# Kernel tuning notes

Measured on AMD Instinct MI355X. Metric: run time of the kernel, lower is better.

The kernel has to match this reference:

```python
import jax, jax.numpy as jnp
import numpy as np

B_, L, DM = 2, 1024, 1024
D_STATE, D_CONV, EXPAND = 16, 4, 2
DI = EXPAND * DM          # 2048 inner dim
DTR = DM // 16            # 64 dt rank


def setup_inputs() -> dict:
    key = jax.random.key(0)
    ks = jax.random.split(key, 16)
    g = lambda k, shp, s: jax.random.normal(k, shp, jnp.float32) * s
    inp = {
        "x": g(ks[0], (B_, L, DM), 1.0),
        "ln_g": jnp.ones((DM,), jnp.float32),
        "ln_b": jnp.zeros((DM,), jnp.float32),
        "in_proj_w": g(ks[1], (2 * DI, DM), (2.0 / (DM + 2 * DI)) ** 0.5),
        "conv_w": g(ks[2], (DI, 1, D_CONV), (2.0 / D_CONV) ** 0.5),
        "conv_b": jnp.zeros((DI,), jnp.float32),
        "dtin_w": g(ks[3], (DTR, DI), (2.0 / (DI + DTR)) ** 0.5),
        "dtin_b": jnp.zeros((DTR,), jnp.float32),
        "dt_w": g(ks[4], (DI, DTR), DTR ** -0.5),
        "dt_b": jnp.log(jnp.expm1(jax.random.uniform(ks[5], (DI,), jnp.float32, 1e-3, 0.1))),  # inverse-softplus of dt in [dt_min, dt_max]
        "B_w": g(ks[6], (D_STATE, DI), DI ** -0.5),
        "C_w": g(ks[7], (D_STATE, DI), DI ** -0.5),
        "A_log": jnp.log(jnp.broadcast_to(jnp.arange(1, D_STATE + 1, dtype=jnp.float32), (DI, D_STATE))),
        "D": jnp.ones((DI,), jnp.float32),
        "out_w": g(ks[8], (DM, DI), (2.0 / (DM + DI)) ** 0.5),
    }
    return inp


def _layernorm(x, g, b, eps=1e-5):
    mu = jnp.mean(x, -1, keepdims=True)
    var = jnp.mean(jnp.square(x - mu), -1, keepdims=True)
    return (x - mu) * jax.lax.rsqrt(var + eps) * g + b


def _selective_scan(u, dt, Bm, Cm, A, Dp):
    # u,dt: (b,l,di); Bm,Cm: (b,l,n); A: (di,n)
    def step(h, inp):
        dt_t, B_t, C_t, u_t = inp  # (b,di),(b,n),(b,n),(b,di)
        dA = jnp.exp(dt_t[..., None] * A)                       # (b,di,n)
        h = h * dA + (dt_t * u_t)[..., None] * B_t[:, None, :]   # (b,di,n)
        y = jnp.einsum("bdn,bn->bd", h, C_t)
        return h, y

    tm = lambda a: jnp.swapaxes(a, 0, 1)  # time-major
    h0 = jnp.zeros((u.shape[0], u.shape[2], A.shape[1]), u.dtype)
    _, ys = jax.lax.scan(step, h0, (tm(dt), tm(Bm), tm(Cm), tm(u)))
    return jnp.swapaxes(ys, 0, 1) + u * Dp  # (b,l,di)


def reference(x, ln_g, ln_b, in_proj_w, conv_w, conv_b, dtin_w, dtin_b,
              dt_w, dt_b, B_w, C_w, A_log, D, out_w):
    residual = x
    xn = _layernorm(x, ln_g, ln_b)
    xz = xn @ in_proj_w.T                       # (b,l,2*di)
    x_proj, z = jnp.split(xz, 2, axis=-1)
    # causal depthwise conv1d (left pad d_conv-1, truncate to seq_len)
    xp = jnp.pad(x_proj, ((0, 0), (D_CONV - 1, 0), (0, 0)))
    x_conv = conv_b
    for k in range(D_CONV):
        x_conv = x_conv + conv_w[:, 0, k] * xp[:, k:k + L, :]
    x_conv = jax.nn.silu(x_conv)
    dt_in = x_conv @ dtin_w.T + dtin_b          # (b,l,dtr)
    dt = jax.nn.softplus(dt_in @ dt_w.T + dt_b) # (b,l,di)
    Bm = x_conv @ B_w.T                         # (b,l,n)
    Cm = x_conv @ C_w.T
    A = -jnp.exp(A_log)                         # (di,n)
    y = _selective_scan(x_conv, dt, Bm, Cm, A, D)
    y = y * jax.nn.silu(z)
    return y @ out_w.T + residual
```

## Files before the change

kernel.cpp:

```cpp
#include <hip/hip_runtime.h>
#include <hip/hip_bf16.h>
#include <cstdint>

#define BL    2
#define LSEQ  1024
#define DMOD  1024
#define DIN   2048
#define NST   16
#define DTRK  64
#define MR    (BL*LSEQ)

#define CCH 16
#define TCH 64
#define KSPLIT 8

typedef __bf16 bf16x8 __attribute__((ext_vector_type(8)));
typedef float  f32x4  __attribute__((ext_vector_type(4)));

#if __has_builtin(__builtin_amdgcn_exp2f)
#define EXP2F(x) __builtin_amdgcn_exp2f(x)
#else
#define EXP2F(x) exp2f(x)
#endif
#define LOG2E 1.4426950408889634f

__device__ __forceinline__ void glds16(const void* g, const void* l) {
    __builtin_amdgcn_global_load_lds(
        (__attribute__((address_space(1))) void*)(uintptr_t)(g),
        (__attribute__((address_space(3))) void*)(uint32_t)(uintptr_t)(l),
        16, 0, 0);
}

__device__ __forceinline__ __bf16 f2b(float f) {
    __hip_bfloat16 t = __float2bfloat16(f);
    return *(__bf16*)&t;
}

template <int MODE, int TM, int TN, int BK>
__global__ __launch_bounds__(256, 3) void gemm_bt(
    const __hip_bfloat16* __restrict__ A, int lda,
    const __hip_bfloat16* __restrict__ Bw, int ldb,
    int M, int N, int Ksl,
    void* __restrict__ e0, void* __restrict__ e1,
    const float* __restrict__ bias, const float* __restrict__ bias2,
    const float* __restrict__ Af)
{
    constexpr bool FUSE = (MODE == 0);
    static_assert(!FUSE || BK == 64, "fused conv epilogue assumes BK=64");
    static_assert(MODE != 2 || BK == 64, "MODE 2 staging assumes BK=64");
    constexpr int WM = TM / 2, WN = TN / 2;
    constexpr int MT = WM / 16, NT = WN / 16;
    constexpr int C8 = BK / 8;
    constexpr int RPP = 256 / C8;
    constexpr int PA = TM / RPP, PB = TN / RPP;
    __shared__ __align__(16) __hip_bfloat16 sA[2][TM * BK];
    __shared__ __align__(16) __hip_bfloat16 sB[2][TN * BK];
    __shared__ __align__(16) __hip_bfloat16 sH[2][(FUSE ? 16 : 1) * 64];

    auto SW = [](int row) { return (BK == 32) ? ((row >> 1) & 3) : (row & 7); };

    int bx = blockIdx.x, by = blockIdx.y;
    if ((gridDim.y & 7) == 0) {
        const int bid = blockIdx.x + gridDim.x * blockIdx.y;
        const int xcd = bid & 7, s = bid >> 3;
        bx = s % gridDim.x;
        by = (s / gridDim.x) * 8 + xcd;
    }
    const int m0 = by * TM;
    const int n0 = bx * TN;
    const int k0 = blockIdx.z * Ksl;
    const int tid = threadIdx.x;
    const int w = tid >> 6, lane = tid & 63;
    const int wm = (w >> 1) * WM, wn = (w & 1) * WN;
    const int lrow = lane & 15, lq = lane >> 4;

    const int r0 = tid / C8;
    const int q = ((tid % C8) - SW(r0)) & (C8 - 1);
    const __hip_bfloat16* pa[PA];
    const __hip_bfloat16* pb[PB];
    if constexpr (MODE != 2) {
#pragma unroll
        for (int p = 0; p < PA; p++) pa[p] = A + (size_t)(m0 + r0 + RPP * p) * lda + k0 + q * 8;
    }
#pragma unroll
    for (int p = 0; p < PB; p++) pb[p] = Bw + (size_t)(n0 + r0 + RPP * p) * ldb + k0 + q * 8;

    auto stageA2 = [&](int buf, int kb) {
        if constexpr (MODE == 2) {
#pragma unroll
            for (int p = 0; p < PA; p++) {
                const int rr = r0 + RPP * p;
                const float* src = Af + (size_t)(m0 + rr) * 64 + kb * BK + q * 8;
                const float4 f0 = *(const float4*)src;
                const float4 f1 = *(const float4*)(src + 4);
                const float4 b0 = *(const float4*)&bias2[q * 8];
                const float4 b1 = *(const float4*)&bias2[q * 8 + 4];
                bf16x8 o;
                o[0] = f2b(f0.x + b0.x); o[1] = f2b(f0.y + b0.y);
                o[2] = f2b(f0.z + b0.z); o[3] = f2b(f0.w + b0.w);
                o[4] = f2b(f1.x + b1.x); o[5] = f2b(f1.y + b1.y);
                o[6] = f2b(f1.z + b1.z); o[7] = f2b(f1.w + b1.w);
                *(bf16x8*)&sA[buf][(tid + 256 * p) * 8] = o;
            }
        }
    };

    const bool isX = FUSE && (n0 < DIN);
    const __hip_bfloat16* ph = nullptr;
    if (FUSE) {
        const int rh = tid >> 3;
        const int qh = ((tid & 7) - (rh & 7)) & 7;
        ph = A + (size_t)(m0 - 16 + rh) * lda + k0 + qh * 8;
    }

    f32x4 acc[MT][NT];
#pragma unroll
    for (int i = 0; i < MT; i++)
#pragma unroll
        for (int j = 0; j < NT; j++) { acc[i][j][0]=0.f; acc[i][j][1]=0.f; acc[i][j][2]=0.f; acc[i][j][3]=0.f; }
    f32x4 hacc[FUSE ? NT : 1];
    if (FUSE)
#pragma unroll
        for (int j = 0; j < NT; j++) { hacc[j][0]=0.f; hacc[j][1]=0.f; hacc[j][2]=0.f; hacc[j][3]=0.f; }

    const int nk = Ksl / BK;
    if constexpr (MODE == 2) stageA2(0, 0);
    else {
#pragma unroll
        for (int p = 0; p < PA; p++) glds16(pa[p], &sA[0][(tid + 256 * p) * 8]);
    }
#pragma unroll
    for (int p = 0; p < PB; p++) glds16(pb[p], &sB[0][(tid + 256 * p) * 8]);
    if (isX && tid < 128) glds16(ph, &sH[0][tid * 8]);

    for (int kb = 0; kb < nk; ++kb) {
        const int cur = kb & 1, nxt = cur ^ 1;
        __syncthreads();
        if (kb + 1 < nk) {
            if constexpr (MODE == 2) stageA2(nxt, kb + 1);
            else {
#pragma unroll
                for (int p = 0; p < PA; p++) { pa[p] += BK; glds16(pa[p], &sA[nxt][(tid + 256 * p) * 8]); }
            }
#pragma unroll
            for (int p = 0; p < PB; p++) { pb[p] += BK; glds16(pb[p], &sB[nxt][(tid + 256 * p) * 8]); }
            if (isX && tid < 128) { ph += BK; glds16(ph, &sH[nxt][tid * 8]); }
        }
#pragma unroll
        for (int s = 0; s < BK / 32; s++) {
            bf16x8 af[MT], bb[NT];
#pragma unroll
            for (int mt = 0; mt < MT; mt++) {
                const int row = wm + mt * 16 + lrow;
                const int pc = ((s * 4 + lq) + SW(row)) & (C8 - 1);
                af[mt] = *(const bf16x8*)&sA[cur][row * BK + pc * 8];
            }
#pragma unroll
            for (int nt = 0; nt < NT; nt++) {
                const int row = wn + nt * 16 + lrow;
                const int pc = ((s * 4 + lq) + SW(row)) & (C8 - 1);
                bb[nt] = *(const bf16x8*)&sB[cur][row * BK + pc * 8];
            }
#pragma unroll
            for (int mt = 0; mt < MT; mt++)
#pragma unroll
                for (int nt = 0; nt < NT; nt++)
                    acc[mt][nt] = __builtin_amdgcn_mfma_f32_16x16x32_bf16(af[mt], bb[nt], acc[mt][nt], 0, 0, 0);
            if (isX && w < 2) {
                const int pcH = ((s * 4 + lq) + (lrow & 7)) & 7;
                const bf16x8 afh = *(const bf16x8*)&sH[cur][lrow * 64 + pcH * 8];
#pragma unroll
                for (int nt = 0; nt < NT; nt++)
                    hacc[nt] = __builtin_amdgcn_mfma_f32_16x16x32_bf16(afh, bb[nt], hacc[nt], 0, 0, 0);
            }
        }
    }

    if (MODE == 0 && isX) {
        __syncthreads();
        __hip_bfloat16* tile = (__hip_bfloat16*)&sB[0][0];
        constexpr int TS = TN + 8;
#pragma unroll
        for (int mt = 0; mt < MT; mt++)
#pragma unroll
            for (int nt = 0; nt < NT; nt++) {
                const int col = wn + nt * 16 + lrow;
#pragma unroll
                for (int r = 0; r < 4; r++)
                    tile[(16 + wm + mt * 16 + lq * 4 + r) * TS + col] = __float2bfloat16(acc[mt][nt][r]);
            }
        if (w < 2) {
#pragma unroll
            for (int nt = 0; nt < NT; nt++) {
                const int col = wn + nt * 16 + lrow;
#pragma unroll
                for (int r = 0; r < 4; r++)
                    tile[(lq * 4 + r) * TS + col] = __float2bfloat16(hacc[nt][r]);
            }
        }
        __syncthreads();
        const int c2 = (tid & 63) * 2;
        const int rg = tid >> 6;
        const int dg = n0 + c2;
        const float4 wA = *(const float4*)&bias[dg * 4];
        const float4 wB = *(const float4*)&bias[dg * 4 + 4];
        const float cbA = bias2[dg], cbB = bias2[dg + 1];
        const int l0 = m0 & (LSEQ - 1);
        const int rbase = rg * 16;
        float a0, a1, a2, b0, b1, b2;
        if (l0 == 0 && rg == 0) {
            a0 = a1 = a2 = b0 = b1 = b2 = 0.f;
        } else {
            const int hr = 16 + rbase - 3;
            a0 = __bfloat162float(tile[(hr + 0) * TS + c2]);
            b0 = __bfloat162float(tile[(hr + 0) * TS + c2 + 1]);
            a1 = __bfloat162float(tile[(hr + 1) * TS + c2]);
            b1 = __bfloat162float(tile[(hr + 1) * TS + c2 + 1]);
            a2 = __bfloat162float(tile[(hr + 2) * TS + c2]);
            b2 = __bfloat162float(tile[(hr + 2) * TS + c2 + 1]);
        }
        __hip_bfloat16* xcbp = (__hip_bfloat16*)e0;
#pragma unroll 4
        for (int i = 0; i < 16; i++) {
            const int row = rbase + i;
            const float a3 = __bfloat162float(tile[(16 + row) * TS + c2]);
            const float b3 = __bfloat162float(tile[(16 + row) * TS + c2 + 1]);
            float sa = cbA + wA.x * a0 + wA.y * a1 + wA.z * a2 + wA.w * a3;
            float sb = cbB + wB.x * b0 + wB.y * b1 + wB.z * b2 + wB.w * b3;
            sa = sa / (1.f + __expf(-sa));
            sb = sb / (1.f + __expf(-sb));
            __hip_bfloat16 ha = __float2bfloat16(sa), hb = __float2bfloat16(sb);
            ushort2 o;
            o.x = (unsigned short)__hip_bfloat16_raw(ha).x;
            o.y = (unsigned short)__hip_bfloat16_raw(hb).x;
            *(ushort2*)&xcbp[(size_t)(m0 + row) * DIN + dg] = o;
            a0 = a1; a1 = a2; a2 = a3;
            b0 = b1; b1 = b2; b2 = b3;
        }
        return;
    }
#pragma unroll
    for (int mt = 0; mt < MT; mt++) {
#pragma unroll
        for (int nt = 0; nt < NT; nt++) {
            const int gn = n0 + wn + nt * 16 + lrow;
            if (gn >= N) continue;
            const int gmb = m0 + wm + mt * 16 + lq * 4;
#pragma unroll
            for (int r = 0; r < 4; r++) {
                const int gm = gmb + r;
                const float v = acc[mt][nt][r];
                if (MODE == 0) {
                    const float s = v / (1.f + __expf(-v));
                    ((__hip_bfloat16*)e1)[(size_t)gm * DIN + (gn - DIN)] = __float2bfloat16(s);
                } else if (MODE == 1) {
                    if (gn < 64)      atomicAdd((float*)e0 + (size_t)gm * 64 + gn, v);
                    else if (gn < 80) atomicAdd((float*)e1 + (size_t)gm * NST + (gn - 64), v);
                    else              atomicAdd((float*)e1 + (size_t)MR * NST + (size_t)gm * NST + (gn - 80), v);
                } else if (MODE == 2) {
                    const float xx = v + bias[gn];
                    const float sp = (xx > 20.f) ? xx : log1pf(__expf(xx));
                    ((__hip_bfloat16*)e0)[(size_t)gm * N + gn] = __float2bfloat16(sp);
                } else {
                    ((float*)e0)[(size_t)gm * N + gn] = v + ((const float*)e1)[(size_t)gm * N + gn];
                }
            }
        }
    }
}

#define NCVT 1654784
#define NZR  49152
__global__ void prep_kernel(const float* __restrict__ x, const float* __restrict__ ln_g,
                            const float* __restrict__ ln_b,
                            const float* __restrict__ w_in, const float* __restrict__ dtin_w,
                            const float* __restrict__ B_w, const float* __restrict__ C_w,
                            const float* __restrict__ dt_w, const float* __restrict__ out_w,
                            __hip_bfloat16* __restrict__ w1b, __hip_bfloat16* __restrict__ wpb,
                            __hip_bfloat16* __restrict__ dtwb, __hip_bfloat16* __restrict__ owb,
                            __hip_bfloat16* __restrict__ xn, float* __restrict__ zblock)
{
    const int b = blockIdx.x;
    const int tid = threadIdx.x;
    if (b < MR) {
        const float4 v = ((const float4*)(x + (size_t)b * DMOD))[tid];
        float s  = v.x + v.y + v.z + v.w;
        float sq = v.x * v.x + v.y * v.y + v.z * v.z + v.w * v.w;
#pragma unroll
        for (int off = 32; off >= 1; off >>= 1) {
            s  += __shfl_down(s, off, 64);
            sq += __shfl_down(sq, off, 64);
        }
        __shared__ float red[8];
        const int w = tid >> 6, lane = tid & 63;
        if (lane == 0) { red[w] = s; red[4 + w] = sq; }
        __syncthreads();
        s  = red[0] + red[1] + red[2] + red[3];
        sq = red[4] + red[5] + red[6] + red[7];
        const float mean = s * (1.f / DMOD);
        const float rstd = rsqrtf(sq * (1.f / DMOD) - mean * mean + 1e-5f);
        const int col = tid * 4;
        const float vv[4] = {v.x, v.y, v.z, v.w};
#pragma unroll
        for (int i = 0; i < 4; i++)
            xn[(size_t)b * DMOD + col + i] =
                __float2bfloat16((vv[i] - mean) * rstd * ln_g[col + i] + ln_b[col + i]);
        return;
    }
    const int nb = gridDim.x - MR;
    for (int v4 = (b - MR) * 256 + tid; v4 < NCVT + NZR; v4 += nb * 256) {
        if (v4 >= NCVT) {
            float4 z; z.x = z.y = z.z = z.w = 0.f;
            ((float4*)zblock)[v4 - NCVT] = z;
            continue;
        }
        const int i = v4 * 4;
        const float* s; __hip_bfloat16* dk;
        if      (i < 4194304) { s = w_in   + i;             dk = w1b  + i; }
        else if (i < 4325376) { s = dtin_w + (i - 4194304); dk = wpb  + (i - 4194304); }
        else if (i < 4358144) { s = B_w    + (i - 4325376); dk = wpb  + 131072 + (i - 4325376); }
        else if (i < 4390912) { s = C_w    + (i - 4358144); dk = wpb  + 163840 + (i - 4358144); }
        else if (i < 4521984) { s = dt_w   + (i - 4390912); dk = dtwb + (i - 4390912); }
        else                  { s = out_w  + (i - 4521984); dk = owb  + (i - 4521984); }
        const float4 f = *(const float4*)s;
        ushort4 o;
        o.x = (unsigned short)(__hip_bfloat16_raw(__float2bfloat16(f.x)).x);
        o.y = (unsigned short)(__hip_bfloat16_raw(__float2bfloat16(f.y)).x);
        o.z = (unsigned short)(__hip_bfloat16_raw(__float2bfloat16(f.z)).x);
        o.w = (unsigned short)(__hip_bfloat16_raw(__float2bfloat16(f.w)).x);
        *(ushort4*)dk = o;
    }
}


__global__ __launch_bounds__(256) void scan_p1(
    const __hip_bfloat16* __restrict__ dt, const __hip_bfloat16* __restrict__ u,
    const float* __restrict__ Bm, const float* __restrict__ A_log,
    float* __restrict__ Aprod, float* __restrict__ Bacc)
{
    __shared__ float sB[TCH * NST];
    const int blk = blockIdx.x;
    const int bb = blk / (CCH * 16), c = (blk >> 4) & (CCH - 1), dtile = blk & 15;
    const int tid = threadIdx.x;
    const int nh = tid & 1, dl = tid >> 1;
    const int d = dtile * 128 + dl;
    const int row0 = bb * LSEQ + c * TCH;

#pragma unroll
    for (int k = 0; k < (TCH * NST) / 256; k++)
        sB[tid + 256 * k] = Bm[(size_t)row0 * NST + tid + 256 * k];
    __syncthreads();

    float a2[8];
    {
        const float4 al0 = *(const float4*)&A_log[(size_t)d * NST + nh * 8];
        const float4 al1 = *(const float4*)&A_log[(size_t)d * NST + nh * 8 + 4];
        a2[0] = -__expf(al0.x) * LOG2E; a2[1] = -__expf(al0.y) * LOG2E;
        a2[2] = -__expf(al0.z) * LOG2E; a2[3] = -__expf(al0.w) * LOG2E;
        a2[4] = -__expf(al1.x) * LOG2E; a2[5] = -__expf(al1.y) * LOG2E;
        a2[6] = -__expf(al1.z) * LOG2E; a2[7] = -__expf(al1.w) * LOG2E;
    }
    const __hip_bfloat16* pdt = dt + (size_t)row0 * DIN + d;
    const __hip_bfloat16* pu  = u  + (size_t)row0 * DIN + d;
    float h[8], Ap[8];
#pragma unroll
    for (int j = 0; j < 8; j++) { h[j] = 0.f; Ap[j] = 1.f; }

#pragma unroll 4
    for (int t = 0; t < TCH; t++) {
        const float dtv = __bfloat162float(pdt[t * DIN]);
        const float uv  = __bfloat162float(pu[t * DIN]);
        const float du = dtv * uv;
        float bv[8];
        *(float4*)&bv[0] = *(const float4*)&sB[t * NST + nh * 8];
        *(float4*)&bv[4] = *(const float4*)&sB[t * NST + nh * 8 + 4];
#pragma unroll
        for (int j = 0; j < 8; j++) {
            const float e = EXP2F(dtv * a2[j]);
            Ap[j] *= e;
            h[j] = h[j] * e + du * bv[j];
        }
    }
    const size_t idx = (((size_t)bb * CCH + c) * DIN + d) * NST + nh * 8;
    *(float4*)&Aprod[idx]     = make_float4(Ap[0], Ap[1], Ap[2], Ap[3]);
    *(float4*)&Aprod[idx + 4] = make_float4(Ap[4], Ap[5], Ap[6], Ap[7]);
    *(float4*)&Bacc[idx]      = make_float4(h[0], h[1], h[2], h[3]);
    *(float4*)&Bacc[idx + 4]  = make_float4(h[4], h[5], h[6], h[7]);
}

__global__ __launch_bounds__(256) void scan_p2(
    const float* __restrict__ Aprod, const float* __restrict__ Bacc,
    float* __restrict__ hstart)
{
    const int i = blockIdx.x * 256 + threadIdx.x;
    const int bb = i >> 15;
    const int dn = i & 32767;
    const size_t base = (((size_t)bb * CCH) << 15) + dn;
    float ap[CCH], bc[CCH];
#pragma unroll
    for (int c = 0; c < CCH; c++) {
        ap[c] = Aprod[base + ((size_t)c << 15)];
        bc[c] = Bacc[base + ((size_t)c << 15)];
    }
    float hs = 0.f;
#pragma unroll
    for (int c = 0; c < CCH; c++) {
        hstart[base + ((size_t)c << 15)] = hs;
        hs = fmaf(ap[c], hs, bc[c]);
    }
}

__global__ __launch_bounds__(256) void scan_p3(
    const __hip_bfloat16* __restrict__ dt, const __hip_bfloat16* __restrict__ u,
    const float* __restrict__ Bm, const float* __restrict__ Cm,
    const float* __restrict__ A_log, const float* __restrict__ Dp,
    const __hip_bfloat16* __restrict__ zs, const float* __restrict__ hstart,
    __hip_bfloat16* __restrict__ y)
{
    __shared__ float sB[TCH * NST], sC[TCH * NST];
    const int blk = blockIdx.x;
    const int bb = blk / (CCH * 16), c = (blk >> 4) & (CCH - 1), dtile = blk & 15;
    const int tid = threadIdx.x;
    const int nh = tid & 1, dl = tid >> 1;
    const int d = dtile * 128 + dl;
    const int row0 = bb * LSEQ + c * TCH;

#pragma unroll
    for (int k = 0; k < (TCH * NST) / 256; k++) {
        sB[tid + 256 * k] = Bm[(size_t)row0 * NST + tid + 256 * k];
        sC[tid + 256 * k] = Cm[(size_t)row0 * NST + tid + 256 * k];
    }
    __syncthreads();

    float a2[8];
    {
        const float4 al0 = *(const float4*)&A_log[(size_t)d * NST + nh * 8];
        const float4 al1 = *(const float4*)&A_log[(size_t)d * NST + nh * 8 + 4];
        a2[0] = -__expf(al0.x) * LOG2E; a2[1] = -__expf(al0.y) * LOG2E;
        a2[2] = -__expf(al0.z) * LOG2E; a2[3] = -__expf(al0.w) * LOG2E;
        a2[4] = -__expf(al1.x) * LOG2E; a2[5] = -__expf(al1.y) * LOG2E;
        a2[6] = -__expf(al1.z) * LOG2E; a2[7] = -__expf(al1.w) * LOG2E;
    }
    const float Dd = Dp[d];
    const size_t idx = (((size_t)bb * CCH + c) * DIN + d) * NST + nh * 8;
    float h[8];
    *(float4*)&h[0] = *(const float4*)&hstart[idx];
    *(float4*)&h[4] = *(const float4*)&hstart[idx + 4];

    const __hip_bfloat16* pdt = dt + (size_t)row0 * DIN + d;
    const __hip_bfloat16* pu  = u  + (size_t)row0 * DIN + d;
    const __hip_bfloat16* pz  = zs + (size_t)row0 * DIN + d;
    __hip_bfloat16* py = y + (size_t)row0 * DIN + d;

#pragma unroll 2
    for (int t = 0; t < TCH; t++) {
        const float dtv = __bfloat162float(pdt[t * DIN]);
        const float uv  = __bfloat162float(pu[t * DIN]);
        const float du = dtv * uv;
        float bv[8], cv[8];
        *(float4*)&bv[0] = *(const float4*)&sB[t * NST + nh * 8];
        *(float4*)&bv[4] = *(const float4*)&sB[t * NST + nh * 8 + 4];
        *(float4*)&cv[0] = *(const float4*)&sC[t * NST + nh * 8];
        *(float4*)&cv[4] = *(const float4*)&sC[t * NST + nh * 8 + 4];
        float yp = 0.f;
#pragma unroll
        for (int j = 0; j < 8; j++) {
            const float e = EXP2F(dtv * a2[j]);
            h[j] = h[j] * e + du * bv[j];
            yp += h[j] * cv[j];
        }
        yp += __shfl_xor(yp, 1, 64);
        if (nh == 0) {
            const float zv = __bfloat162float(pz[t * DIN]);
            py[t * DIN] = __float2bfloat16((yp + uv * Dd) * zv);
        }
    }
}

extern "C" void kernel_launch(void* const* d_in, const int* in_sizes, int n_in,
                              void* d_out, int out_size, void* d_ws, size_t ws_size,
                              hipStream_t stream) {
    const float* x      = (const float*)d_in[0];
    const float* ln_g   = (const float*)d_in[1];
    const float* ln_b   = (const float*)d_in[2];
    const float* w_in   = (const float*)d_in[3];
    const float* conv_w = (const float*)d_in[4];
    const float* conv_b = (const float*)d_in[5];
    const float* dtin_w = (const float*)d_in[6];
    const float* dtin_b = (const float*)d_in[7];
    const float* dt_w   = (const float*)d_in[8];
    const float* dt_b   = (const float*)d_in[9];
    const float* B_w    = (const float*)d_in[10];
    const float* C_w    = (const float*)d_in[11];
    const float* A_log  = (const float*)d_in[12];
    const float* Dp     = (const float*)d_in[13];
    const float* out_w  = (const float*)d_in[14];
    float* out = (float*)d_out;

    char* ws = (char*)d_ws;
    auto alloc = [&](size_t bytes) { char* p = ws; ws += (bytes + 255) & ~255ull; return p; };
    __hip_bfloat16* w1b   = (__hip_bfloat16*)alloc((size_t)4096 * 1024 * 2);
    __hip_bfloat16* wpb   = (__hip_bfloat16*)alloc((size_t)96 * 2048 * 2);
    __hip_bfloat16* dtwb  = (__hip_bfloat16*)alloc((size_t)2048 * 64 * 2);
    __hip_bfloat16* owb   = (__hip_bfloat16*)alloc((size_t)1024 * 2048 * 2);
    __hip_bfloat16* xnb   = (__hip_bfloat16*)alloc((size_t)MR * DMOD * 2);
    __hip_bfloat16* zs    = (__hip_bfloat16*)alloc((size_t)MR * DIN * 2);
    __hip_bfloat16* xcb   = (__hip_bfloat16*)alloc((size_t)MR * DIN * 2);
    __hip_bfloat16* dtb   = (__hip_bfloat16*)alloc((size_t)MR * DIN * 2);
    __hip_bfloat16* yb    = (__hip_bfloat16*)alloc((size_t)MR * DIN * 2);
    float*          zblock= (float*)alloc((size_t)196608 * 4);
    float*          Aprod = (float*)alloc((size_t)BL * CCH * DIN * NST * 4);
    float*          Bacc  = (float*)alloc((size_t)BL * CCH * DIN * NST * 4);
    float*          hstart= (float*)alloc((size_t)BL * CCH * DIN * NST * 4);

    float* fdtin = zblock;
    float* Bmf   = zblock + 131072;

    prep_kernel<<<MR + 896, 256, 0, stream>>>(x, ln_g, ln_b, w_in, dtin_w, B_w, C_w, dt_w,
                                              out_w, w1b, wpb, dtwb, owb, xnb, zblock);

    gemm_bt<0, 64, 128, 64><<<dim3(32, 32, 1), 256, 0, stream>>>(
        xnb, 1024, w1b, 1024, MR, 4096, 1024, xcb, zs, conv_w, conv_b, nullptr);

    gemm_bt<1, 64, 128, 64><<<dim3(1, 32, KSPLIT), 256, 0, stream>>>(
        xcb, 2048, wpb, 2048, MR, 96, 2048 / KSPLIT, fdtin, Bmf, nullptr, nullptr, nullptr);

    gemm_bt<2, 64, 128, 64><<<dim3(16, 32, 1), 256, 0, stream>>>(
        nullptr, 0, dtwb, 64, MR, DIN, 64, dtb, nullptr, dt_b, dtin_b, fdtin);

    scan_p1<<<BL * CCH * 16, 256, 0, stream>>>(dtb, xcb, Bmf, A_log, Aprod, Bacc);
    scan_p2<<<BL * DIN * NST / 256, 256, 0, stream>>>(Aprod, Bacc, hstart);
    scan_p3<<<BL * CCH * 16, 256, 0, stream>>>(dtb, xcb, Bmf, Bmf + (size_t)MR * NST,
                                               A_log, Dp, zs, hstart, yb);

    gemm_bt<3, 64, 64, 64><<<dim3(16, 32, 1), 256, 0, stream>>>(
        yb, 2048, owb, 2048, MR, DMOD, 2048, out, (void*)x, nullptr, nullptr, nullptr);
}
```

Before: 247.9 us.

## Stage scan dt/u/z tiles in LDS and shorten chunk length in chunked scan

The scan kernels now copy the per-chunk dt, u and z tiles into shared memory with async global-to-LDS 16-byte loads, instead of each thread doing strided 2-byte global loads every timestep. Outputs y are gathered in LDS and written back as coalesced 16-byte vector stores. The chunk length goes from 64 to 32 and the chunk count from 16 to 32, which doubles the blocks for more parallelism but lengthens the sequential cross-chunk prefix pass. The barrier is moved after the A_log/hstart loads so that latency overlaps the async copies.

Result: faster. 222.0 us (-10.4%).

```diff
diff --git a/kernel.cpp b/kernel.cpp
--- a/kernel.cpp
+++ b/kernel.cpp
@@ -10,8 +10,8 @@
 #define DTRK  64
 #define MR    (BL*LSEQ)
 
-#define CCH 16
-#define TCH 64
+#define CCH 32
+#define TCH 32
 #define KSPLIT 8
 
 typedef __bf16 bf16x8 __attribute__((ext_vector_type(8)));
@@ -339,17 +339,29 @@
     float* __restrict__ Aprod, float* __restrict__ Bacc)
 {
     __shared__ float sB[TCH * NST];
+    __shared__ __align__(16) __hip_bfloat16 sDT[TCH * 128];
+    __shared__ __align__(16) __hip_bfloat16 sU [TCH * 128];
     const int blk = blockIdx.x;
     const int bb = blk / (CCH * 16), c = (blk >> 4) & (CCH - 1), dtile = blk & 15;
     const int tid = threadIdx.x;
     const int nh = tid & 1, dl = tid >> 1;
     const int d = dtile * 128 + dl;
+    const int d0 = dtile * 128;
     const int row0 = bb * LSEQ + c * TCH;
 
+    {
+        const int r = tid >> 4, cq = (tid & 15) * 8;
+        const __hip_bfloat16* gdt = dt + (size_t)row0 * DIN + d0;
+        const __hip_bfloat16* gu  = u  + (size_t)row0 * DIN + d0;
+#pragma unroll
+        for (int p = 0; p < TCH / 16; p++) {
+            glds16(gdt + (size_t)(r + 16 * p) * DIN + cq, &sDT[(r + 16 * p) * 128 + cq]);
+            glds16(gu  + (size_t)(r + 16 * p) * DIN + cq, &sU [(r + 16 * p) * 128 + cq]);
+        }
+    }
 #pragma unroll
     for (int k = 0; k < (TCH * NST) / 256; k++)
         sB[tid + 256 * k] = Bm[(size_t)row0 * NST + tid + 256 * k];
-    __syncthreads();
 
     float a2[8];
     {
@@ -360,16 +372,16 @@
         a2[4] = -__expf(al1.x) * LOG2E; a2[5] = -__expf(al1.y) * LOG2E;
         a2[6] = -__expf(al1.z) * LOG2E; a2[7] = -__expf(al1.w) * LOG2E;
     }
-    const __hip_bfloat16* pdt = dt + (size_t)row0 * DIN + d;
-    const __hip_bfloat16* pu  = u  + (size_t)row0 * DIN + d;
+    __syncthreads();
+
     float h[8], Ap[8];
 #pragma unroll
     for (int j = 0; j < 8; j++) { h[j] = 0.f; Ap[j] = 1.f; }
 
 #pragma unroll 4
     for (int t = 0; t < TCH; t++) {
-        const float dtv = __bfloat162float(pdt[t * DIN]);
-        const float uv  = __bfloat162float(pu[t * DIN]);
+        const float dtv = __bfloat162float(sDT[t * 128 + dl]);
+        const float uv  = __bfloat162float(sU [t * 128 + dl]);
         const float du = dtv * uv;
         float bv[8];
         *(float4*)&bv[0] = *(const float4*)&sB[t * NST + nh * 8];
@@ -418,19 +430,35 @@
     __hip_bfloat16* __restrict__ y)
 {
     __shared__ float sB[TCH * NST], sC[TCH * NST];
+    __shared__ __align__(16) __hip_bfloat16 sDT[TCH * 128];
+    __shared__ __align__(16) __hip_bfloat16 sU [TCH * 128];
+    __shared__ __align__(16) __hip_bfloat16 sZ [TCH * 128];
+    __shared__ __align__(16) __hip_bfloat16 sY [TCH * 128];
     const int blk = blockIdx.x;
     const int bb = blk / (CCH * 16), c = (blk >> 4) & (CCH - 1), dtile = blk & 15;
     const int tid = threadIdx.x;
     const int nh = tid & 1, dl = tid >> 1;
     const int d = dtile * 128 + dl;
+    const int d0 = dtile * 128;
     const int row0 = bb * LSEQ + c * TCH;
 
+    {
+        const int r = tid >> 4, cq = (tid & 15) * 8;
+        const __hip_bfloat16* gdt = dt + (size_t)row0 * DIN + d0;
+        const __hip_bfloat16* gu  = u  + (size_t)row0 * DIN + d0;
+        const __hip_bfloat16* gz  = zs + (size_t)row0 * DIN + d0;
+#pragma unroll
+        for (int p = 0; p < TCH / 16; p++) {
+            glds16(gdt + (size_t)(r + 16 * p) * DIN + cq, &sDT[(r + 16 * p) * 128 + cq]);
+            glds16(gu  + (size_t)(r + 16 * p) * DIN + cq, &sU [(r + 16 * p) * 128 + cq]);
+            glds16(gz  + (size_t)(r + 16 * p) * DIN + cq, &sZ [(r + 16 * p) * 128 + cq]);
+        }
+    }
 #pragma unroll
     for (int k = 0; k < (TCH * NST) / 256; k++) {
         sB[tid + 256 * k] = Bm[(size_t)row0 * NST + tid + 256 * k];
         sC[tid + 256 * k] = Cm[(size_t)row0 * NST + tid + 256 * k];
     }
-    __syncthreads();
 
     float a2[8];
     {
@@ -446,16 +474,12 @@
     float h[8];
     *(float4*)&h[0] = *(const float4*)&hstart[idx];
     *(float4*)&h[4] = *(const float4*)&hstart[idx + 4];
-
-    const __hip_bfloat16* pdt = dt + (size_t)row0 * DIN + d;
-    const __hip_bfloat16* pu  = u  + (size_t)row0 * DIN + d;
-    const __hip_bfloat16* pz  = zs + (size_t)row0 * DIN + d;
-    __hip_bfloat16* py = y + (size_t)row0 * DIN + d;
-
-#pragma unroll 2
+    __syncthreads();
+
+#pragma unroll 4
     for (int t = 0; t < TCH; t++) {
-        const float dtv = __bfloat162float(pdt[t * DIN]);
-        const float uv  = __bfloat162float(pu[t * DIN]);
+        const float dtv = __bfloat162float(sDT[t * 128 + dl]);
+        const float uv  = __bfloat162float(sU [t * 128 + dl]);
         const float du = dtv * uv;
         float bv[8], cv[8];
         *(float4*)&bv[0] = *(const float4*)&sB[t * NST + nh * 8];
@@ -471,9 +495,18 @@
         }
         yp += __shfl_xor(yp, 1, 64);
         if (nh == 0) {
-            const float zv = __bfloat162float(pz[t * DIN]);
-            py[t * DIN] = __float2bfloat16((yp + uv * Dd) * zv);
-        }
+            const float zv = __bfloat162float(sZ[t * 128 + dl]);
+            sY[t * 128 + dl] = __float2bfloat16((yp + uv * Dd) * zv);
+        }
+    }
+    __syncthreads();
+    {
+        const int r = tid >> 4, cq = (tid & 15) * 8;
+        __hip_bfloat16* gy = y + (size_t)row0 * DIN + d0;
+#pragma unroll
+        for (int p = 0; p < TCH / 16; p++)
+            *(bf16x8*)(gy + (size_t)(r + 16 * p) * DIN + cq) =
+                *(const bf16x8*)&sY[(r + 16 * p) * 128 + cq];
     }
 }
 
```
